# Kernel tuning notes

Hardware: AMD Instinct MI355X
Metric: run time of the kernel (lower is better)

## Reference

```python
import jax, jax.numpy as jnp
import numpy as np

D, K = 128, 32
B, H, W = 16, 64, 64


def setup_inputs() -> dict:
    key = jax.random.key(0)
    k1, k2, k3 = jax.random.split(key, 3)
    x = jax.random.normal(k1, (B, D, H, W), dtype=jnp.float32)
    std1 = 1.0 / (K * D) ** 0.5
    codewords = jax.random.uniform(k2, (K, D), minval=-std1, maxval=std1, dtype=jnp.float32)
    scale = jax.random.uniform(k3, (K,), minval=-1.0, maxval=0.0, dtype=jnp.float32)
    return {"x": x, "codewords": codewords, "scale": scale}


def reference(x, codewords, scale):
    b = x.shape[0]
    # (B, D, H, W) -> (B, N, D)
    X = x.reshape(b, D, -1).transpose(0, 2, 1)
    # scaled L2: SL[b,n,k] = scale[k] * ||X[b,n] - C[k]||^2, expanded to avoid (B,N,K,D)
    x2 = jnp.sum(X * X, axis=-1)                      # (B, N)
    c2 = jnp.sum(codewords * codewords, axis=-1)      # (K,)
    xc = jnp.einsum('bnd,kd->bnk', X, codewords)      # (B, N, K)
    SL = scale[None, None, :] * (x2[:, :, None] - 2.0 * xc + c2[None, None, :])
    A = jax.nn.softmax(SL, axis=2)                    # (B, N, K)
    # E[b,k,d] = sum_n A[b,n,k] * (X[b,n,d] - C[k,d])
    E = jnp.einsum('bnk,bnd->bkd', A, X) - jnp.sum(A, axis=1)[:, :, None] * codewords[None, :, :]
    return E
```

## Files before the change

kernel.cpp:

```cpp
#include <hip/hip_runtime.h>
#include <hip/hip_bf16.h>


#define D_   128
#define K_   32
#define NPB  64
#define NTOT 4096

typedef __attribute__((ext_vector_type(8))) short bf16x8;
typedef __attribute__((ext_vector_type(4))) float f32x4;
typedef __attribute__((ext_vector_type(4))) short short4v;

__device__ __forceinline__ short f2b(float f) {
  return (short)__builtin_bit_cast(unsigned short, __float2bfloat16(f));
}

__global__ __launch_bounds__(256, 4) void enc_kernel(
    const float* __restrict__ x,
    const float* __restrict__ cw,
    const float* __restrict__ scale,
    float* __restrict__ out)
{
  __shared__ __align__(16) short sNb[NPB * D_];
  __shared__ __align__(16) short sDb[D_ * NPB];
  __shared__ __align__(16) short sAb[K_ * NPB];
  __shared__ __align__(16) float sX2w[NPB * 4];
  __shared__ float sasum[K_];

  const int t  = threadIdx.x;
  const int w  = t >> 6;
  const int l  = t & 63;
  const int lr = l & 15;
  const int lg = l >> 4;
  const int b  = blockIdx.x >> 6;
  const int n0 = (blockIdx.x & 63) * NPB;

  if (t < K_) sasum[t] = 0.0f;

  const int n4s = t & 15;
  const int d0  = (t >> 4) * 8;
  const float* xb = x + (size_t)b * D_ * NTOT + n0;
  float4 xs[8];
  #pragma unroll
  for (int j = 0; j < 8; ++j)
    xs[j] = *reinterpret_cast<const float4*>(xb + (size_t)(d0 + j) * NTOT + n4s * 4);

  short xb16[8][4];
  #pragma unroll
  for (int j = 0; j < 8; ++j) {
    xb16[j][0] = f2b(xs[j].x); xb16[j][1] = f2b(xs[j].y);
    xb16[j][2] = f2b(xs[j].z); xb16[j][3] = f2b(xs[j].w);
  }
  float p2[4] = {0.f, 0.f, 0.f, 0.f};
  #pragma unroll
  for (int j = 0; j < 8; ++j) {
    p2[0] = fmaf(xs[j].x, xs[j].x, p2[0]);
    p2[1] = fmaf(xs[j].y, xs[j].y, p2[1]);
    p2[2] = fmaf(xs[j].z, xs[j].z, p2[2]);
    p2[3] = fmaf(xs[j].w, xs[j].w, p2[3]);
  }
  #pragma unroll
  for (int i = 0; i < 4; ++i) {
    p2[i] += __shfl_xor(p2[i], 16);
    p2[i] += __shfl_xor(p2[i], 32);
  }
  if (lg == 0) {
    #pragma unroll
    for (int i = 0; i < 4; ++i) sX2w[(n4s * 4 + i) * 4 + w] = p2[i];
  }
  #pragma unroll
  for (int i = 0; i < 4; ++i) {
    int n = n4s * 4 + i;
    bf16x8 pk;
    #pragma unroll
    for (int j = 0; j < 8; ++j) pk[j] = xb16[j][i];
    int phys = ((d0 >> 3) ^ (n & 15)) & 15;
    *reinterpret_cast<bf16x8*>(&sNb[n * D_ + phys * 8]) = pk;
  }
  #pragma unroll
  for (int j = 0; j < 8; ++j) {
    int d = d0 + j;
    int phys = ((n4s >> 1) ^ (d & 7) ^ ((d >> 3) & 7)) & 7;
    short4v pk4 = {xb16[j][0], xb16[j][1], xb16[j][2], xb16[j][3]};
    *reinterpret_cast<short4v*>(&sDb[d * NPB + phys * 8 + (n4s & 1) * 4]) = pk4;
  }

  bf16x8 bC[2][4];
  float c2p0 = 0.f, c2p1 = 0.f;
  #pragma unroll
  for (int kt = 0; kt < 2; ++kt) {
    const float* crow = cw + (lr + 16 * kt) * D_ + lg * 8;
    #pragma unroll
    for (int s = 0; s < 4; ++s) {
      float4 v0 = *reinterpret_cast<const float4*>(crow + 32 * s);
      float4 v1 = *reinterpret_cast<const float4*>(crow + 32 * s + 4);
      float vv[8] = {v0.x, v0.y, v0.z, v0.w, v1.x, v1.y, v1.z, v1.w};
      bf16x8 f;
      float cs = 0.f;
      #pragma unroll
      for (int j = 0; j < 8; ++j) { f[j] = f2b(vv[j]); cs = fmaf(vv[j], vv[j], cs); }
      bC[kt][s] = f;
      if (kt == 0) c2p0 += cs; else c2p1 += cs;
    }
  }
  c2p0 += __shfl_xor(c2p0, 16); c2p0 += __shfl_xor(c2p0, 32);
  c2p1 += __shfl_xor(c2p1, 16); c2p1 += __shfl_xor(c2p1, 32);
  const float sc0 = scale[lr];
  const float sc1 = scale[lr + 16];
  __syncthreads();

  const int m0 = w * 16;
  const int nrow = m0 + lr;
  f32x4 p0 = {0.f, 0.f, 0.f, 0.f}, p1 = {0.f, 0.f, 0.f, 0.f};
  #pragma unroll
  for (int s = 0; s < 4; ++s) {
    int dblk = 4 * s + lg;
    bf16x8 af = *reinterpret_cast<const bf16x8*>(
        &sNb[nrow * D_ + ((dblk ^ lr) & 15) * 8]);
    p0 = __builtin_amdgcn_mfma_f32_16x16x32_bf16(af, bC[0][s], p0, 0, 0, 0);
    p1 = __builtin_amdgcn_mfma_f32_16x16x32_bf16(af, bC[1][s], p1, 0, 0, 0);
  }
  float x2r[4];
  #pragma unroll
  for (int r = 0; r < 4; ++r) {
    float4 v = *reinterpret_cast<const float4*>(&sX2w[(m0 + lg * 4 + r) * 4]);
    x2r[r] = (v.x + v.y) + (v.z + v.w);
  }

  float a0[4], a1[4], mr[4], sr[4];
  #pragma unroll
  for (int r = 0; r < 4; ++r) {
    float sl0 = sc0 * (x2r[r] - 2.f * p0[r] + c2p0);
    float sl1 = sc1 * (x2r[r] - 2.f * p1[r] + c2p1);
    a0[r] = sl0; a1[r] = sl1;
    mr[r] = fmaxf(sl0, sl1);
  }
  #pragma unroll
  for (int dlt = 1; dlt <= 8; dlt <<= 1)
    #pragma unroll
    for (int r = 0; r < 4; ++r) mr[r] = fmaxf(mr[r], __shfl_xor(mr[r], dlt));
  #pragma unroll
  for (int r = 0; r < 4; ++r) {
    a0[r] = __expf(a0[r] - mr[r]);
    a1[r] = __expf(a1[r] - mr[r]);
    sr[r] = a0[r] + a1[r];
  }
  #pragma unroll
  for (int dlt = 1; dlt <= 8; dlt <<= 1)
    #pragma unroll
    for (int r = 0; r < 4; ++r) sr[r] += __shfl_xor(sr[r], dlt);
  #pragma unroll
  for (int r = 0; r < 4; ++r) {
    float inv = 1.0f / sr[r];
    a0[r] *= inv; a1[r] *= inv;
  }

  float as0 = a0[0] + a0[1] + a0[2] + a0[3];
  float as1 = a1[0] + a1[1] + a1[2] + a1[3];
  as0 += __shfl_xor(as0, 16); as0 += __shfl_xor(as0, 32);
  as1 += __shfl_xor(as1, 16); as1 += __shfl_xor(as1, 32);
  if (lg == 0) {
    atomicAdd(&sasum[lr], as0);
    atomicAdd(&sasum[lr + 16], as1);
  }
  #pragma unroll
  for (int r = 0; r < 4; ++r) {
    int n = m0 + lg * 4 + r;
    sAb[lr * 64 + (n ^ ((lr & 7) << 3))] = f2b(a0[r]);
    sAb[(lr + 16) * 64 + (n ^ (((lr + 16) & 7) << 3))] = f2b(a1[r]);
  }
  __syncthreads();

  bf16x8 aA[2][2];
  #pragma unroll
  for (int mt = 0; mt < 2; ++mt) {
    int k = mt * 16 + lr;
    #pragma unroll
    for (int s = 0; s < 2; ++s) {
      int nb = 32 * s + lg * 8;
      aA[mt][s] = *reinterpret_cast<const bf16x8*>(
          &sAb[k * 64 + (nb ^ ((k & 7) << 3))]);
    }
  }
  float asv[2][4];
  #pragma unroll
  for (int mt = 0; mt < 2; ++mt)
    #pragma unroll
    for (int r = 0; r < 4; ++r) asv[mt][r] = sasum[mt * 16 + lg * 4 + r];
  f32x4 acc[2][2];
  #pragma unroll
  for (int mt = 0; mt < 2; ++mt)
    #pragma unroll
    for (int dti = 0; dti < 2; ++dti) {
      int d = (2 * w + dti) * 16 + lr;
      #pragma unroll
      for (int r = 0; r < 4; ++r) {
        int k = mt * 16 + lg * 4 + r;
        acc[mt][dti][r] = -asv[mt][r] * cw[k * D_ + d];
      }
    }
  #pragma unroll
  for (int s = 0; s < 2; ++s) {
    #pragma unroll
    for (int dti = 0; dti < 2; ++dti) {
      int d = (2 * w + dti) * 16 + lr;
      int phys = (((4 * s + lg) ^ (d & 7) ^ ((d >> 3) & 7)) & 7);
      bf16x8 bf = *reinterpret_cast<const bf16x8*>(&sDb[d * NPB + phys * 8]);
      acc[0][dti] = __builtin_amdgcn_mfma_f32_16x16x32_bf16(aA[0][s], bf, acc[0][dti], 0, 0, 0);
      acc[1][dti] = __builtin_amdgcn_mfma_f32_16x16x32_bf16(aA[1][s], bf, acc[1][dti], 0, 0, 0);
    }
  }
  float* op = out + (size_t)b * K_ * D_;
  #pragma unroll
  for (int mt = 0; mt < 2; ++mt)
    #pragma unroll
    for (int dti = 0; dti < 2; ++dti) {
      int d = (2 * w + dti) * 16 + lr;
      #pragma unroll
      for (int r = 0; r < 4; ++r) {
        int k = mt * 16 + lg * 4 + r;
        unsafeAtomicAdd(&op[k * D_ + d], acc[mt][dti][r]);
      }
    }
}

extern "C" void kernel_launch(void* const* d_in, const int* in_sizes, int n_in,
                              void* d_out, int out_size, void* d_ws, size_t ws_size,
                              hipStream_t stream) {
  const float* x  = (const float*)d_in[0];
  const float* cw = (const float*)d_in[1];
  const float* sc = (const float*)d_in[2];
  float* out = (float*)d_out;
  const int B = in_sizes[0] / (D_ * NTOT);
  hipMemsetAsync(d_out, 0, (size_t)out_size * sizeof(float), stream);
  enc_kernel<<<dim3(B * (NTOT / NPB)), dim3(256), 0, stream>>>(x, cw, sc, out);
}
```

Measured before the change: 91.13 us.

## Process two point tiles per block with prefetch of the next tile

Each block now handles 128 points as two 64-point tiles instead of one. The second tile's global loads are issued before the first tile's compute, and its accumulators stay in registers, so global atomics are halved. The codeword fragments are loaded once per block rather than per 64 points. This adds extra barriers and register pressure, and the launch bound is lowered to 2 blocks per SM. The grid is also halved, which may reduce the parallelism available to hide latency.

```diff
diff --git a/kernel.cpp b/kernel.cpp
--- a/kernel.cpp
+++ b/kernel.cpp
@@ -15,7 +15,7 @@
   return (short)__builtin_bit_cast(unsigned short, __float2bfloat16(f));
 }
 
-__global__ __launch_bounds__(256, 4) void enc_kernel(
+__global__ __launch_bounds__(256, 2) void enc_kernel(
     const float* __restrict__ x,
     const float* __restrict__ cw,
     const float* __restrict__ scale,
@@ -32,58 +32,12 @@
   const int l  = t & 63;
   const int lr = l & 15;
   const int lg = l >> 4;
-  const int b  = blockIdx.x >> 6;
-  const int n0 = (blockIdx.x & 63) * NPB;
-
-  if (t < K_) sasum[t] = 0.0f;
+  const int b  = blockIdx.x >> 5;
+  const int nbase = (blockIdx.x & 31) * 128;
 
   const int n4s = t & 15;
   const int d0  = (t >> 4) * 8;
-  const float* xb = x + (size_t)b * D_ * NTOT + n0;
-  float4 xs[8];
-  #pragma unroll
-  for (int j = 0; j < 8; ++j)
-    xs[j] = *reinterpret_cast<const float4*>(xb + (size_t)(d0 + j) * NTOT + n4s * 4);
-
-  short xb16[8][4];
-  #pragma unroll
-  for (int j = 0; j < 8; ++j) {
-    xb16[j][0] = f2b(xs[j].x); xb16[j][1] = f2b(xs[j].y);
-    xb16[j][2] = f2b(xs[j].z); xb16[j][3] = f2b(xs[j].w);
-  }
-  float p2[4] = {0.f, 0.f, 0.f, 0.f};
-  #pragma unroll
-  for (int j = 0; j < 8; ++j) {
-    p2[0] = fmaf(xs[j].x, xs[j].x, p2[0]);
-    p2[1] = fmaf(xs[j].y, xs[j].y, p2[1]);
-    p2[2] = fmaf(xs[j].z, xs[j].z, p2[2]);
-    p2[3] = fmaf(xs[j].w, xs[j].w, p2[3]);
-  }
-  #pragma unroll
-  for (int i = 0; i < 4; ++i) {
-    p2[i] += __shfl_xor(p2[i], 16);
-    p2[i] += __shfl_xor(p2[i], 32);
-  }
-  if (lg == 0) {
-    #pragma unroll
-    for (int i = 0; i < 4; ++i) sX2w[(n4s * 4 + i) * 4 + w] = p2[i];
-  }
-  #pragma unroll
-  for (int i = 0; i < 4; ++i) {
-    int n = n4s * 4 + i;
-    bf16x8 pk;
-    #pragma unroll
-    for (int j = 0; j < 8; ++j) pk[j] = xb16[j][i];
-    int phys = ((d0 >> 3) ^ (n & 15)) & 15;
-    *reinterpret_cast<bf16x8*>(&sNb[n * D_ + phys * 8]) = pk;
-  }
-  #pragma unroll
-  for (int j = 0; j < 8; ++j) {
-    int d = d0 + j;
-    int phys = ((n4s >> 1) ^ (d & 7) ^ ((d >> 3) & 7)) & 7;
-    short4v pk4 = {xb16[j][0], xb16[j][1], xb16[j][2], xb16[j][3]};
-    *reinterpret_cast<short4v*>(&sDb[d * NPB + phys * 8 + (n4s & 1) * 4]) = pk4;
-  }
+  const float* xb = x + (size_t)b * D_ * NTOT + nbase;
 
   bf16x8 bC[2][4];
   float c2p0 = 0.f, c2p1 = 0.f;
@@ -107,87 +61,176 @@
   c2p1 += __shfl_xor(c2p1, 16); c2p1 += __shfl_xor(c2p1, 32);
   const float sc0 = scale[lr];
   const float sc1 = scale[lr + 16];
+
+  float4 xs[8];
+  #pragma unroll
+  for (int j = 0; j < 8; ++j)
+    xs[j] = *reinterpret_cast<const float4*>(xb + (size_t)(d0 + j) * NTOT + n4s * 4);
+  if (t < K_) sasum[t] = 0.0f;
+
+  #define STAGE_TILE()                                                        \
+  {                                                                           \
+    short xb16[8][4];                                                         \
+    _Pragma("unroll")                                                         \
+    for (int j = 0; j < 8; ++j) {                                             \
+      xb16[j][0] = f2b(xs[j].x); xb16[j][1] = f2b(xs[j].y);                   \
+      xb16[j][2] = f2b(xs[j].z); xb16[j][3] = f2b(xs[j].w);                   \
+    }                                                                         \
+    float p2[4] = {0.f, 0.f, 0.f, 0.f};                                       \
+    _Pragma("unroll")                                                         \
+    for (int j = 0; j < 8; ++j) {                                             \
+      p2[0] = fmaf(xs[j].x, xs[j].x, p2[0]);                                  \
+      p2[1] = fmaf(xs[j].y, xs[j].y, p2[1]);                                  \
+      p2[2] = fmaf(xs[j].z, xs[j].z, p2[2]);                                  \
+      p2[3] = fmaf(xs[j].w, xs[j].w, p2[3]);                                  \
+    }                                                                         \
+    _Pragma("unroll")                                                         \
+    for (int i = 0; i < 4; ++i) {                                             \
+      p2[i] += __shfl_xor(p2[i], 16);                                         \
+      p2[i] += __shfl_xor(p2[i], 32);                                         \
+    }                                                                         \
+    if (lg == 0) {                                                            \
+      _Pragma("unroll")                                                       \
+      for (int i = 0; i < 4; ++i) sX2w[(n4s * 4 + i) * 4 + w] = p2[i];        \
+    }                                                                         \
+    _Pragma("unroll")                                                         \
+    for (int i = 0; i < 4; ++i) {                                             \
+      int n = n4s * 4 + i;                                                    \
+      bf16x8 pk;                                                              \
+      _Pragma("unroll")                                                       \
+      for (int j = 0; j < 8; ++j) pk[j] = xb16[j][i];                         \
+      int phys = ((d0 >> 3) ^ (n & 15)) & 15;                                 \
+      *reinterpret_cast<bf16x8*>(&sNb[n * D_ + phys * 8]) = pk;               \
+    }                                                                         \
+    _Pragma("unroll")                                                         \
+    for (int j = 0; j < 8; ++j) {                                             \
+      int d = d0 + j;                                                         \
+      int phys = ((n4s >> 1) ^ (d & 7) ^ ((d >> 3) & 7)) & 7;                 \
+      short4v pk4 = {xb16[j][0], xb16[j][1], xb16[j][2], xb16[j][3]};         \
+      *reinterpret_cast<short4v*>(&sDb[d * NPB + phys * 8 + (n4s & 1) * 4]) = pk4; \
+    }                                                                         \
+  }
+
+  STAGE_TILE();
   __syncthreads();
 
   const int m0 = w * 16;
   const int nrow = m0 + lr;
-  f32x4 p0 = {0.f, 0.f, 0.f, 0.f}, p1 = {0.f, 0.f, 0.f, 0.f};
-  #pragma unroll
-  for (int s = 0; s < 4; ++s) {
-    int dblk = 4 * s + lg;
-    bf16x8 af = *reinterpret_cast<const bf16x8*>(
-        &sNb[nrow * D_ + ((dblk ^ lr) & 15) * 8]);
-    p0 = __builtin_amdgcn_mfma_f32_16x16x32_bf16(af, bC[0][s], p0, 0, 0, 0);
-    p1 = __builtin_amdgcn_mfma_f32_16x16x32_bf16(af, bC[1][s], p1, 0, 0, 0);
-  }
-  float x2r[4];
-  #pragma unroll
-  for (int r = 0; r < 4; ++r) {
-    float4 v = *reinterpret_cast<const float4*>(&sX2w[(m0 + lg * 4 + r) * 4]);
-    x2r[r] = (v.x + v.y) + (v.z + v.w);
-  }
-
-  float a0[4], a1[4], mr[4], sr[4];
-  #pragma unroll
-  for (int r = 0; r < 4; ++r) {
-    float sl0 = sc0 * (x2r[r] - 2.f * p0[r] + c2p0);
-    float sl1 = sc1 * (x2r[r] - 2.f * p1[r] + c2p1);
-    a0[r] = sl0; a1[r] = sl1;
-    mr[r] = fmaxf(sl0, sl1);
-  }
-  #pragma unroll
-  for (int dlt = 1; dlt <= 8; dlt <<= 1)
-    #pragma unroll
-    for (int r = 0; r < 4; ++r) mr[r] = fmaxf(mr[r], __shfl_xor(mr[r], dlt));
-  #pragma unroll
-  for (int r = 0; r < 4; ++r) {
-    a0[r] = __expf(a0[r] - mr[r]);
-    a1[r] = __expf(a1[r] - mr[r]);
-    sr[r] = a0[r] + a1[r];
-  }
-  #pragma unroll
-  for (int dlt = 1; dlt <= 8; dlt <<= 1)
-    #pragma unroll
-    for (int r = 0; r < 4; ++r) sr[r] += __shfl_xor(sr[r], dlt);
-  #pragma unroll
-  for (int r = 0; r < 4; ++r) {
-    float inv = 1.0f / sr[r];
-    a0[r] *= inv; a1[r] *= inv;
-  }
-
-  float as0 = a0[0] + a0[1] + a0[2] + a0[3];
-  float as1 = a1[0] + a1[1] + a1[2] + a1[3];
-  as0 += __shfl_xor(as0, 16); as0 += __shfl_xor(as0, 32);
-  as1 += __shfl_xor(as1, 16); as1 += __shfl_xor(as1, 32);
-  if (lg == 0) {
-    atomicAdd(&sasum[lr], as0);
-    atomicAdd(&sasum[lr + 16], as1);
-  }
-  #pragma unroll
-  for (int r = 0; r < 4; ++r) {
-    int n = m0 + lg * 4 + r;
-    sAb[lr * 64 + (n ^ ((lr & 7) << 3))] = f2b(a0[r]);
-    sAb[(lr + 16) * 64 + (n ^ (((lr + 16) & 7) << 3))] = f2b(a1[r]);
-  }
-  __syncthreads();
-
-  bf16x8 aA[2][2];
+  f32x4 acc[2][2];
+  float asvT[2][4];
   #pragma unroll
   for (int mt = 0; mt < 2; ++mt) {
-    int k = mt * 16 + lr;
+    #pragma unroll
+    for (int dti = 0; dti < 2; ++dti) acc[mt][dti] = (f32x4){0.f, 0.f, 0.f, 0.f};
+    #pragma unroll
+    for (int r = 0; r < 4; ++r) asvT[mt][r] = 0.f;
+  }
+
+  #pragma unroll
+  for (int tile = 0; tile < 2; ++tile) {
+    if (tile == 0) {
+      #pragma unroll
+      for (int j = 0; j < 8; ++j)
+        xs[j] = *reinterpret_cast<const float4*>(
+            xb + 64 + (size_t)(d0 + j) * NTOT + n4s * 4);
+    }
+
+    f32x4 p0 = {0.f, 0.f, 0.f, 0.f}, p1 = {0.f, 0.f, 0.f, 0.f};
+    #pragma unroll
+    for (int s = 0; s < 4; ++s) {
+      int dblk = 4 * s + lg;
+      bf16x8 af = *reinterpret_cast<const bf16x8*>(
+          &sNb[nrow * D_ + ((dblk ^ lr) & 15) * 8]);
+      p0 = __builtin_amdgcn_mfma_f32_16x16x32_bf16(af, bC[0][s], p0, 0, 0, 0);
+      p1 = __builtin_amdgcn_mfma_f32_16x16x32_bf16(af, bC[1][s], p1, 0, 0, 0);
+    }
+    float x2r[4];
+    #pragma unroll
+    for (int r = 0; r < 4; ++r) {
+      float4 v = *reinterpret_cast<const float4*>(&sX2w[(m0 + lg * 4 + r) * 4]);
+      x2r[r] = (v.x + v.y) + (v.z + v.w);
+    }
+
+    float a0[4], a1[4], mr[4], sr[4];
+    #pragma unroll
+    for (int r = 0; r < 4; ++r) {
+      float sl0 = sc0 * (x2r[r] - 2.f * p0[r] + c2p0);
+      float sl1 = sc1 * (x2r[r] - 2.f * p1[r] + c2p1);
+      a0[r] = sl0; a1[r] = sl1;
+      mr[r] = fmaxf(sl0, sl1);
+    }
+    #pragma unroll
+    for (int dlt = 1; dlt <= 8; dlt <<= 1)
+      #pragma unroll
+      for (int r = 0; r < 4; ++r) mr[r] = fmaxf(mr[r], __shfl_xor(mr[r], dlt));
+    #pragma unroll
+    for (int r = 0; r < 4; ++r) {
+      a0[r] = __expf(a0[r] - mr[r]);
+      a1[r] = __expf(a1[r] - mr[r]);
+      sr[r] = a0[r] + a1[r];
+    }
+    #pragma unroll
+    for (int dlt = 1; dlt <= 8; dlt <<= 1)
+      #pragma unroll
+      for (int r = 0; r < 4; ++r) sr[r] += __shfl_xor(sr[r], dlt);
+    #pragma unroll
+    for (int r = 0; r < 4; ++r) {
+      float inv = 1.0f / sr[r];
+      a0[r] *= inv; a1[r] *= inv;
+    }
+
+    float as0 = a0[0] + a0[1] + a0[2] + a0[3];
+    float as1 = a1[0] + a1[1] + a1[2] + a1[3];
+    as0 += __shfl_xor(as0, 16); as0 += __shfl_xor(as0, 32);
+    as1 += __shfl_xor(as1, 16); as1 += __shfl_xor(as1, 32);
+    if (lg == 0) {
+      atomicAdd(&sasum[lr], as0);
+      atomicAdd(&sasum[lr + 16], as1);
+    }
+    #pragma unroll
+    for (int r = 0; r < 4; ++r) {
+      int n = m0 + lg * 4 + r;
+      sAb[lr * 64 + (n ^ ((lr & 7) << 3))] = f2b(a0[r]);
+      sAb[(lr + 16) * 64 + (n ^ (((lr + 16) & 7) << 3))] = f2b(a1[r]);
+    }
+    __syncthreads();
+
+    bf16x8 aA[2][2];
+    #pragma unroll
+    for (int mt = 0; mt < 2; ++mt) {
+      int k = mt * 16 + lr;
+      #pragma unroll
+      for (int s = 0; s < 2; ++s) {
+        int nb = 32 * s + lg * 8;
+        aA[mt][s] = *reinterpret_cast<const bf16x8*>(
+            &sAb[k * 64 + (nb ^ ((k & 7) << 3))]);
+      }
+    }
+    #pragma unroll
+    for (int mt = 0; mt < 2; ++mt)
+      #pragma unroll
+      for (int r = 0; r < 4; ++r) asvT[mt][r] += sasum[mt * 16 + lg * 4 + r];
     #pragma unroll
     for (int s = 0; s < 2; ++s) {
-      int nb = 32 * s + lg * 8;
-      aA[mt][s] = *reinterpret_cast<const bf16x8*>(
-          &sAb[k * 64 + (nb ^ ((k & 7) << 3))]);
-    }
-  }
-  float asv[2][4];
-  #pragma unroll
-  for (int mt = 0; mt < 2; ++mt)
-    #pragma unroll
-    for (int r = 0; r < 4; ++r) asv[mt][r] = sasum[mt * 16 + lg * 4 + r];
-  f32x4 acc[2][2];
+      #pragma unroll
+      for (int dti = 0; dti < 2; ++dti) {
+        int d = (2 * w + dti) * 16 + lr;
+        int phys = (((4 * s + lg) ^ (d & 7) ^ ((d >> 3) & 7)) & 7);
+        bf16x8 bf = *reinterpret_cast<const bf16x8*>(&sDb[d * NPB + phys * 8]);
+        acc[0][dti] = __builtin_amdgcn_mfma_f32_16x16x32_bf16(aA[0][s], bf, acc[0][dti], 0, 0, 0);
+        acc[1][dti] = __builtin_amdgcn_mfma_f32_16x16x32_bf16(aA[1][s], bf, acc[1][dti], 0, 0, 0);
+      }
+    }
+    __syncthreads();
+
+    if (tile == 0) {
+      if (t < K_) sasum[t] = 0.0f;
+      STAGE_TILE();
+      __syncthreads();
+    }
+  }
+
+  float* op = out + (size_t)b * K_ * D_;
   #pragma unroll
   for (int mt = 0; mt < 2; ++mt)
     #pragma unroll
@@ -196,30 +239,8 @@
       #pragma unroll
       for (int r = 0; r < 4; ++r) {
         int k = mt * 16 + lg * 4 + r;
-        acc[mt][dti][r] = -asv[mt][r] * cw[k * D_ + d];
-      }
-    }
-  #pragma unroll
-  for (int s = 0; s < 2; ++s) {
-    #pragma unroll
-    for (int dti = 0; dti < 2; ++dti) {
-      int d = (2 * w + dti) * 16 + lr;
-      int phys = (((4 * s + lg) ^ (d & 7) ^ ((d >> 3) & 7)) & 7);
-      bf16x8 bf = *reinterpret_cast<const bf16x8*>(&sDb[d * NPB + phys * 8]);
-      acc[0][dti] = __builtin_amdgcn_mfma_f32_16x16x32_bf16(aA[0][s], bf, acc[0][dti], 0, 0, 0);
-      acc[1][dti] = __builtin_amdgcn_mfma_f32_16x16x32_bf16(aA[1][s], bf, acc[1][dti], 0, 0, 0);
-    }
-  }
-  float* op = out + (size_t)b * K_ * D_;
-  #pragma unroll
-  for (int mt = 0; mt < 2; ++mt)
-    #pragma unroll
-    for (int dti = 0; dti < 2; ++dti) {
-      int d = (2 * w + dti) * 16 + lr;
-      #pragma unroll
-      for (int r = 0; r < 4; ++r) {
-        int k = mt * 16 + lg * 4 + r;
-        unsafeAtomicAdd(&op[k * D_ + d], acc[mt][dti][r]);
+        float v = acc[mt][dti][r] - asvT[mt][r] * cw[k * D_ + d];
+        unsafeAtomicAdd(&op[k * D_ + d], v);
       }
     }
 }
@@ -233,5 +254,5 @@
   float* out = (float*)d_out;
   const int B = in_sizes[0] / (D_ * NTOT);
   hipMemsetAsync(d_out, 0, (size_t)out_size * sizeof(float), stream);
-  enc_kernel<<<dim3(B * (NTOT / NPB)), dim3(256), 0, stream>>>(x, cw, sc, out);
+  enc_kernel<<<dim3(B * 32), dim3(256), 0, stream>>>(x, cw, sc, out);
 }
```

Measured after the change: 89.77 us. No clear change (-1.5%).
